# Kernel tuning notes

Hardware: AMD Instinct MI355X
Metric: run time of the kernel (lower is better)

Reference implementation:

```python
import jax, jax.numpy as jnp
import numpy as np

DIM = 256
NUM_HEADS = 4
HEAD_DIM = DIM // NUM_HEADS


def setup_inputs() -> dict:
    key = jax.random.key(0)
    ks = jax.random.split(key, 8)
    B, N, C = 4, 2048, DIM
    x = jax.random.normal(ks[0], (B, N, C), dtype=jnp.float32)
    R = jax.random.normal(ks[1], (B, 3, 3), dtype=jnp.float32)
    P = jax.random.normal(ks[2], (N, 3), dtype=jnp.float32)
    s = 1.0 / np.sqrt(C)
    qkv_w = jax.random.normal(ks[3], (3 * C, C), dtype=jnp.float32) * s
    qkv_b = jax.random.normal(ks[4], (3 * C,), dtype=jnp.float32) * 0.02
    proj_w = jax.random.normal(ks[5], (C, C), dtype=jnp.float32) * s
    proj_b = jax.random.normal(ks[6], (C,), dtype=jnp.float32) * 0.02
    pos_scale = jnp.asarray(1.0, dtype=jnp.float32)
    return {"x": x, "R": R, "P": P, "qkv_w": qkv_w, "qkv_b": qkv_b,
            "proj_w": proj_w, "proj_b": proj_b, "pos_scale": pos_scale}


def reference(x, R, P, qkv_w, qkv_b, proj_w, proj_b, pos_scale):
    B, N, C = x.shape
    H, D = NUM_HEADS, HEAD_DIM
    scale = D ** -0.5
    # qkv: (B,N,3C) -> (3,B,H,N,D)
    qkv = (x @ qkv_w.T + qkv_b).reshape(B, N, 3, H, D).transpose(2, 0, 3, 1, 4)
    q, k, v = qkv[0], qkv[1], qkv[2]
    # attention logits (B,H,N,N)
    attn = jnp.einsum('bhid,bhjd->bhij', q, k) * scale
    # positional bias: RP = (R @ P^T)^T -> (B,N,3); bias_ij = dot(RP_i, P_j)
    RP = jnp.einsum('bab,jb->bja', R, P) if False else jnp.einsum('bca,ja->bjc', jnp.swapaxes(R, 1, 2), P)
    RP = jnp.einsum('bcd,jd->bjc', R, P)  # (B,N,3): (R @ P.T).T
    bias = jnp.einsum('bik,jk->bij', RP, P)[:, None, :, :] * pos_scale  # (B,1,N,N) broadcast over heads
    attn = jax.nn.softmax(attn + bias, axis=-1)
    out = jnp.einsum('bhij,bhjd->bhid', attn, v)  # (B,H,N,D)
    out = out.transpose(0, 2, 1, 3).reshape(B, N, C)
    out = out @ proj_w.T + proj_b
    return out
```

## Files before the change

kernel.cpp:

```cpp
#include <hip/hip_runtime.h>
#include <hip/hip_bf16.h>

#define B_ 4
#define N_ 2048
#define C_ 256
#define H_ 4
#define D_ 64

typedef __attribute__((ext_vector_type(8))) short bf16x8;
typedef __attribute__((ext_vector_type(4))) float f32x4;

#define LOG2E 1.4426950408889634f

static __device__ inline unsigned short f2bf(float f) {
    unsigned u = __builtin_bit_cast(unsigned, f);
    unsigned r = (u + 0x7fffu + ((u >> 16) & 1u)) >> 16;
    return (unsigned short)r;
}
static __device__ inline float bf2f(unsigned short h) {
    unsigned u = ((unsigned)h) << 16;
    return __builtin_bit_cast(float, u);
}
static __device__ inline unsigned pack2(float a, float b) {
    __hip_bfloat162 h = __float22bfloat162_rn(make_float2(a, b));
    unsigned u;
    __builtin_memcpy(&u, &h, 4);
    return u;
}
static __device__ inline bf16x8 ld_frag(const unsigned short* p) {
    return __builtin_bit_cast(bf16x8, *(const uint4*)p);
}
static __device__ inline void gload_lds16(const unsigned short* g, unsigned short* l) {
    __builtin_amdgcn_global_load_lds(
        (const __attribute__((address_space(1))) unsigned int*)(g),
        (__attribute__((address_space(3))) unsigned int*)(l),
        16, 0, 0);
}
template<int CTRL>
static __device__ inline float fmax_dpp(float x) {
    int yi = __builtin_amdgcn_update_dpp(0, __builtin_bit_cast(int, x),
                                         CTRL, 0xf, 0xf, true);
    return fmaxf(x, __builtin_bit_cast(float, yi));
}

__global__ __launch_bounds__(256) void cvt_kernel(
    const float* __restrict__ x, const float* __restrict__ qkv_w,
    const float* __restrict__ proj_w, const float* __restrict__ Pm,
    unsigned short* __restrict__ xb, unsigned short* __restrict__ wqb,
    unsigned short* __restrict__ wpb, unsigned short* __restrict__ eb)
{
    const int bid = blockIdx.x, tid = threadIdx.x;
    if (bid >= 1152) {
        const int n = (bid - 1152) * 256 + tid;
        const float* pp = Pm + n * 3;
        float p0 = pp[0], p1 = pp[1], p2 = pp[2];
        unsigned u0 = f2bf(p0), u1 = f2bf(p1), u2 = f2bf(p2);
        unsigned v0 = f2bf(p0 - bf2f((unsigned short)u0));
        unsigned v1 = f2bf(p1 - bf2f((unsigned short)u1));
        unsigned v2 = f2bf(p2 - bf2f((unsigned short)u2));
        uint4 lo, hi;
        lo.x = u0 | (u1 << 16); lo.y = u2 | (v0 << 16);
        lo.z = v1 | (v2 << 16); lo.w = u0 | (u1 << 16);
        hi.x = u2; hi.y = 0u; hi.z = 0u; hi.w = 0u;
        *(uint4*)&eb[n * 16 + 0] = lo;
        *(uint4*)&eb[n * 16 + 8] = hi;
        return;
    }
    const float* s; unsigned short* d; int i;
    if (bid < 1024)      { s = x;      d = xb;  i = (bid * 256 + tid) * 8; }
    else if (bid < 1120) { s = qkv_w;  d = wqb; i = ((bid - 1024) * 256 + tid) * 8; }
    else                 { s = proj_w; d = wpb; i = ((bid - 1120) * 256 + tid) * 8; }
    float4 a = *(const float4*)(s + i);
    float4 b = *(const float4*)(s + i + 4);
    uint4 u;
    u.x = pack2(a.x, a.y); u.y = pack2(a.z, a.w);
    u.z = pack2(b.x, b.y); u.w = pack2(b.z, b.w);
    *(uint4*)(d + i) = u;
}

__global__ __launch_bounds__(256) void qkv_gemm(
    const unsigned short* __restrict__ xb, const unsigned short* __restrict__ wb,
    const float* __restrict__ bias, unsigned short* __restrict__ qb,
    unsigned short* __restrict__ kb, unsigned short* __restrict__ vt)
{
    __shared__ __align__(16) unsigned short As[2][128 * 64];
    __shared__ __align__(16) unsigned short Bs[2][128 * 64];
    const int m0 = blockIdx.x * 128, o0 = blockIdx.y * 128;
    const int tid = threadIdx.x;
    const int wave = tid >> 6, lane = tid & 63, quad = lane >> 4, l16 = lane & 15;
    const int wy = wave >> 1, wx = wave & 1;
    const int x7 = l16 & 7;
    const int rl = lane >> 3, sl = lane & 7;
    const int swz = (sl ^ rl) * 8;

    const unsigned short* aq0 = &xb[(size_t)(m0 + 32 * wave + rl) * 256 + swz];
    const unsigned short* bq0 = &wb[(size_t)(o0 + 32 * wave + rl) * 256 + swz];

    auto ISSUE = [&](int buf, int k0) {
        unsigned short* ad = &As[buf][(32 * wave) * 64];
        unsigned short* bd = &Bs[buf][(32 * wave) * 64];
        #pragma unroll
        for (int i = 0; i < 4; ++i) {
            gload_lds16(aq0 + (size_t)(8 * i) * 256 + k0, ad + (8 * i) * 64);
            gload_lds16(bq0 + (size_t)(8 * i) * 256 + k0, bd + (8 * i) * 64);
        }
    };

    f32x4 acc[4][4];
    #pragma unroll
    for (int i = 0; i < 4; ++i)
        #pragma unroll
        for (int j = 0; j < 4; ++j) acc[i][j] = (f32x4){0.f, 0.f, 0.f, 0.f};

    ISSUE(0, 0);

    #pragma unroll
    for (int t = 0; t < 4; ++t) {
        const int cur = t & 1;
        asm volatile("s_waitcnt vmcnt(0)" ::: "memory");
        __builtin_amdgcn_s_barrier();
        __builtin_amdgcn_sched_barrier(0);
        if (t < 3) ISSUE(cur ^ 1, (t + 1) * 64);
        __builtin_amdgcn_s_setprio(1);
        #pragma unroll
        for (int ks = 0; ks < 2; ++ks) {
            bf16x8 a[4], b[4];
            #pragma unroll
            for (int mt = 0; mt < 4; ++mt)
                a[mt] = ld_frag(&As[cur][(wy * 64 + mt * 16 + l16) * 64
                                         + (((ks * 4 + quad) ^ x7) * 8)]);
            #pragma unroll
            for (int nt = 0; nt < 4; ++nt)
                b[nt] = ld_frag(&Bs[cur][(wx * 64 + nt * 16 + l16) * 64
                                         + (((ks * 4 + quad) ^ x7) * 8)]);
            #pragma unroll
            for (int mt = 0; mt < 4; ++mt)
                #pragma unroll
                for (int nt = 0; nt < 4; ++nt)
                    acc[mt][nt] = __builtin_amdgcn_mfma_f32_16x16x32_bf16(a[mt], b[nt], acc[mt][nt], 0, 0, 0);
        }
        __builtin_amdgcn_s_setprio(0);
    }

    const int sec = o0 + wx * 64;
    const int three = sec >> 8;
    const int h = (sec >> 6) & 3;
    const int b = m0 >> 11;
    float bv[4];
    #pragma unroll
    for (int nt = 0; nt < 4; ++nt) bv[nt] = bias[sec + nt * 16 + l16];

    if (three == 2) {
        const int n64 = (m0 + wy * 64) & 2047;
        const size_t bh64 = ((size_t)b * H_ + h) * 64;
        #pragma unroll
        for (int nt = 0; nt < 4; ++nt) {
            int d = nt * 16 + l16;
            #pragma unroll
            for (int r = 0; r < 4; ++r) {
                ushort4 v;
                v.x = f2bf(acc[0][nt][r] + bv[nt]);
                v.y = f2bf(acc[1][nt][r] + bv[nt]);
                v.z = f2bf(acc[2][nt][r] + bv[nt]);
                v.w = f2bf(acc[3][nt][r] + bv[nt]);
                *(ushort4*)&vt[(bh64 + d) * N_ + n64 + 16 * quad + 4 * r] = v;
            }
        }
    } else {
        unsigned short* dst = (three == 0) ? qb : kb;
        float sc = (three == 0) ? (0.125f * LOG2E) : 1.0f;
        #pragma unroll
        for (int mt = 0; mt < 4; ++mt)
            #pragma unroll
            for (int r = 0; r < 4; ++r) {
                int n = (m0 + wy * 64 + mt * 16 + quad * 4 + r) & 2047;
                size_t rowbase = (((size_t)b * H_ + h) * N_ + n) * D_;
                #pragma unroll
                for (int nt = 0; nt < 4; ++nt)
                    dst[rowbase + nt * 16 + l16] = f2bf((acc[mt][nt][r] + bv[nt]) * sc);
            }
    }
}

#define LDK 64

__global__ __launch_bounds__(512, 4) void attn_kernel(
    const unsigned short* __restrict__ qb, const unsigned short* __restrict__ kb,
    const unsigned short* __restrict__ vt, const unsigned short* __restrict__ eb,
    const float* __restrict__ Rm, const float* __restrict__ Pm,
    const float* __restrict__ ps_ptr,
    unsigned short* __restrict__ Opart, float* __restrict__ ml)
{
    __shared__ __align__(16) unsigned short Ks[2][64 * LDK];
    __shared__ __align__(16) unsigned short Vs[2][64 * LDK];
    __shared__ __align__(16) unsigned short Ps[128 * LDK];

    const int bh = blockIdx.y;
    const int b = bh >> 2;
    const int i0 = blockIdx.x * 128;
    const int split = blockIdx.z;
    const int tid = threadIdx.x;
    const int wave = tid >> 6, lane = tid & 63;
    const int quad = lane >> 4, l16 = lane & 15;
    const int x7 = l16 & 7;
    const float ps = ps_ptr[0];

    const size_t base = (size_t)bh * N_ * D_;
    const unsigned short* qg = qb + base;
    const unsigned short* kg = kb + base;
    const unsigned short* vg = vt + base;

    const int jbeg = split * (N_ / 2);

    const int rl = lane >> 3, sl = lane & 7;
    const int swz = (sl ^ rl) * 8;
    const unsigned short* kq = kg + (size_t)(jbeg + wave * 8 + rl) * D_ + swz;
    const unsigned short* vq = vg + (size_t)(wave * 8 + rl) * N_ + jbeg + swz;
    const unsigned short* ep = eb + (size_t)(jbeg + l16) * 16 + (quad & 1) * 8;

    auto ISSUE_K = [&](int nb) {
        gload_lds16(kq, &Ks[nb][(wave * 8) * LDK]);
        kq += 64 * D_;
    };
    auto ISSUE_V = [&](int nb) {
        gload_lds16(vq, &Vs[nb][(wave * 8) * LDK]);
        vq += 64;
    };
    auto LOAD_E = [&](bf16x8 (&e)[4]) {
        #pragma unroll
        for (int t = 0; t < 4; ++t) e[t] = ld_frag(ep + t * 256);
        ep += 64 * 16;
    };

    ISSUE_K(0);
    bf16x8 eA[4], eB[4];
    LOAD_E(eA);

    const int qrow = i0 + wave * 16 + l16;
    bf16x8 aq[3];
    #pragma unroll
    for (int ks = 0; ks < 2; ++ks)
        aq[ks] = ld_frag(&qg[(size_t)qrow * D_ + ks * 32 + quad * 8]);

    {
        float p0 = Pm[qrow * 3 + 0], p1 = Pm[qrow * 3 + 1], p2 = Pm[qrow * 3 + 2];
        float sc = ps * LOG2E;
        unsigned short ah[3], al[3];
        #pragma unroll
        for (int c = 0; c < 3; ++c) {
            float a = (Rm[b * 9 + c * 3 + 0] * p0 + Rm[b * 9 + c * 3 + 1] * p1
                     + Rm[b * 9 + c * 3 + 2] * p2) * sc;
            ah[c] = f2bf(a);
            al[c] = f2bf(a - bf2f(ah[c]));
        }
        bf16x8 e = (bf16x8){0,0,0,0,0,0,0,0};
        if (quad == 0) {
            e[0] = (short)ah[0]; e[1] = (short)ah[1]; e[2] = (short)ah[2];
            e[3] = (short)ah[0]; e[4] = (short)ah[1]; e[5] = (short)ah[2];
            e[6] = (short)al[0]; e[7] = (short)al[1];
        } else if (quad == 1) {
            e[0] = (short)al[2];
        }
        aq[2] = e;
    }

    const bf16x8 ones = (bf16x8){0x3F80,0x3F80,0x3F80,0x3F80,0x3F80,0x3F80,0x3F80,0x3F80};

    float m_run = -1e30f;
    f32x4 o_acc[4], lacc;
    #pragma unroll
    for (int t = 0; t < 4; ++t) o_acc[t] = (f32x4){0.f, 0.f, 0.f, 0.f};
    lacc = (f32x4){0.f, 0.f, 0.f, 0.f};

    f32x4 sA[4], sB[4];

    auto S_COMPUTE = [&](f32x4 (&sc)[4], int kb_, bf16x8 (&ec)[4]) {
        __builtin_amdgcn_s_setprio(1);
        #pragma unroll
        for (int t = 0; t < 4; ++t) {
            const int rb = (l16 + 16 * t) * LDK;
            f32x4 c = {0.f, 0.f, 0.f, 0.f};
            #pragma unroll
            for (int ks = 0; ks < 2; ++ks) {
                bf16x8 bk = ld_frag(&Ks[kb_][rb + (((ks * 4 + quad) ^ x7) * 8)]);
                c = __builtin_amdgcn_mfma_f32_16x16x32_bf16(aq[ks], bk, c, 0, 0, 0);
            }
            c = __builtin_amdgcn_mfma_f32_16x16x32_bf16(aq[2], ec[t], c, 0, 0, 0);
            sc[t] = c;
        }
        __builtin_amdgcn_s_setprio(0);
    };

    auto SOFTMAX = [&](f32x4 (&s)[4]) {
        float mt[4];
        #pragma unroll
        for (int t = 0; t < 4; ++t)
            mt[t] = fmaxf(fmaxf(fmaxf(s[t][0], s[t][1]), s[t][2]), s[t][3]);
        float mx = fmaxf(fmaxf(fmaxf(mt[0], mt[1]), mt[2]), mt[3]);
        mx = fmax_dpp<0xB1>(mx);
        mx = fmax_dpp<0x4E>(mx);
        mx = fmax_dpp<0x124>(mx);
        mx = fmax_dpp<0x128>(mx);
        if (__any(mx > m_run + 8.0f)) {
            float mnew = fmaxf(m_run, mx);
            float alpha = exp2f(m_run - mnew);
            #pragma unroll
            for (int t = 0; t < 4; ++t)
                #pragma unroll
                for (int r = 0; r < 4; ++r)
                    o_acc[t][r] *= alpha;
            #pragma unroll
            for (int r = 0; r < 4; ++r) lacc[r] *= alpha;
            m_run = mnew;
        }
        #pragma unroll
        for (int r = 0; r < 4; ++r) {
            float p0 = exp2f(s[0][r] - m_run), p1 = exp2f(s[1][r] - m_run);
            float p2 = exp2f(s[2][r] - m_run), p3 = exp2f(s[3][r] - m_run);
            uint2 w;
            w.x = pack2(p0, p1);
            w.y = pack2(p2, p3);
            const int prow = quad * 4 + r;
            *(uint2*)&Ps[(wave * 16 + prow) * LDK
                         + (((l16 >> 1) ^ (prow & 7)) * 8) + (l16 & 1) * 4] = w;
        }
    };

    auto PV = [&](int vb_) {
        __builtin_amdgcn_s_setprio(1);
        #pragma unroll
        for (int ks = 0; ks < 2; ++ks) {
            bf16x8 ap = ld_frag(&Ps[(wave * 16 + l16) * LDK
                                    + (((ks * 4 + quad) ^ x7) * 8)]);
            #pragma unroll
            for (int t = 0; t < 4; ++t) {
                bf16x8 bv = ld_frag(&Vs[vb_][(l16 + 16 * t) * LDK
                                             + (((ks * 4 + quad) ^ x7) * 8)]);
                o_acc[t] = __builtin_amdgcn_mfma_f32_16x16x32_bf16(ap, bv, o_acc[t], 0, 0, 0);
            }
            lacc = __builtin_amdgcn_mfma_f32_16x16x32_bf16(ap, ones, lacc, 0, 0, 0);
        }
        __builtin_amdgcn_s_setprio(0);
    };

    auto STEP = [&](int cur, bool more, f32x4 (&snew)[4], f32x4 (&sold)[4],
                    bf16x8 (&euse)[4], bf16x8 (&eload)[4]) {
        asm volatile("s_waitcnt vmcnt(0)" ::: "memory");
        __builtin_amdgcn_s_barrier();
        __builtin_amdgcn_sched_barrier(0);
        if (more) ISSUE_K(cur ^ 1);
        ISSUE_V(cur);
        SOFTMAX(sold);
        S_COMPUTE(snew, cur, euse);
        if (more) LOAD_E(eload);
        PV(cur ^ 1);
    };

    asm volatile("s_waitcnt vmcnt(0)" ::: "memory");
    __builtin_amdgcn_s_barrier();
    __builtin_amdgcn_sched_barrier(0);
    ISSUE_K(1);
    ISSUE_V(0);
    S_COMPUTE(sA, 0, eA);
    LOAD_E(eB);

    #pragma unroll 1
    for (int it = 0; it < 7; ++it) {
        STEP(1, true, sB, sA, eB, eA);
        STEP(0, true, sA, sB, eA, eB);
    }
    STEP(1, false, sB, sA, eB, eA);

    asm volatile("s_waitcnt vmcnt(0)" ::: "memory");
    __builtin_amdgcn_s_barrier();
    __builtin_amdgcn_sched_barrier(0);
    SOFTMAX(sB);
    PV(1);

    const size_t pbase = (size_t)(split * 16 + bh) * N_;
    #pragma unroll
    for (int r = 0; r < 4; ++r) {
        int row = i0 + wave * 16 + quad * 4 + r;
        #pragma unroll
        for (int t = 0; t < 4; ++t)
            Opart[(pbase + row) * D_ + l16 + 16 * t] = f2bf(o_acc[t][r]);
        if (l16 == 0) {
            float2* mlp = (float2*)ml;
            mlp[pbase + row] = make_float2(m_run, lacc[r]);
        }
    }
}

__global__ __launch_bounds__(256) void proj_gemm(
    const unsigned short* __restrict__ Opart, const float* __restrict__ ml,
    const unsigned short* __restrict__ wb, const float* __restrict__ bias,
    float* __restrict__ out)
{
    __shared__ __align__(16) unsigned short As[2][64 * 64];
    __shared__ __align__(16) unsigned short Bs[2][64 * 64];
    const int m0 = blockIdx.x * 64, o0 = blockIdx.y * 64;
    const int tid = threadIdx.x;
    const int wave = tid >> 6, lane = tid & 63, quad = lane >> 4, l16 = lane & 15;
    const int x7 = l16 & 7;
    const int rl = lane >> 3, sl = lane & 7;
    const int swz = (sl ^ rl) * 8;
    const float2* mlp = (const float2*)ml;

    const int srow = tid >> 2, sc16 = (tid & 3) * 16;
    const int s0 = (tid & 3) * 2;
    const int sm = m0 + srow, sb = sm >> 11, sn = sm & 2047;

    float wgt[4][2];
    #pragma unroll
    for (int h = 0; h < 4; ++h) {
        size_t r1 = (size_t)(sb * 4 + h) * N_ + sn;
        float2 m0v = mlp[r1], m1v = mlp[r1 + 16 * N_];
        float mm = fmaxf(m0v.x, m1v.x);
        float w0 = exp2f(m0v.x - mm), w1 = exp2f(m1v.x - mm);
        float inv = 1.f / (m0v.y * w0 + m1v.y * w1);
        wgt[h][0] = w0 * inv; wgt[h][1] = w1 * inv;
    }

    const unsigned short* bq0 = &wb[(size_t)(o0 + 16 * wave + rl) * 256 + swz];
    auto ISSUE_B = [&](int buf, int k0) {
        unsigned short* bd = &Bs[buf][(16 * wave) * 64];
        gload_lds16(bq0 + k0,           bd);
        gload_lds16(bq0 + 8 * 256 + k0, bd + 8 * 64);
    };

    union U16 { uint4 u; unsigned short s[8]; };
    U16 ar[2][2];
    auto LOAD_A = [&](int h) {
        size_t r1 = (size_t)(sb * 4 + h) * N_ + sn;
        #pragma unroll
        for (int s = 0; s < 2; ++s) {
            const unsigned short* p = &Opart[(r1 + (size_t)(16 * s) * N_) * D_ + sc16];
            ar[s][0].u = *(const uint4*)(p);
            ar[s][1].u = *(const uint4*)(p + 8);
        }
    };

    ISSUE_B(0, 0);
    LOAD_A(0);

    f32x4 acc[4];
    #pragma unroll
    for (int j = 0; j < 4; ++j) acc[j] = (f32x4){0.f, 0.f, 0.f, 0.f};

    #pragma unroll
    for (int t = 0; t < 4; ++t) {
        const int cur = t & 1;
        {
            float w0 = wgt[t][0], w1 = wgt[t][1];
            #pragma unroll
            for (int j = 0; j < 2; ++j) {
                uint4 mv;
                unsigned* mp = (unsigned*)&mv;
                #pragma unroll
                for (int q = 0; q < 4; ++q) {
                    float lo = bf2f(ar[0][j].s[2*q])   * w0 + bf2f(ar[1][j].s[2*q])   * w1;
                    float hi = bf2f(ar[0][j].s[2*q+1]) * w0 + bf2f(ar[1][j].s[2*q+1]) * w1;
                    mp[q] = pack2(lo, hi);
                }
                *(uint4*)&As[cur][srow * 64 + (((s0 + j) ^ (srow & 7)) * 8)] = mv;
            }
        }
        __syncthreads();
        if (t < 3) {
            ISSUE_B(cur ^ 1, (t + 1) * 64);
            LOAD_A(t + 1);
        }
        __builtin_amdgcn_s_setprio(1);
        #pragma unroll
        for (int ks = 0; ks < 2; ++ks) {
            bf16x8 a = ld_frag(&As[cur][(wave * 16 + l16) * 64
                                        + (((ks * 4 + quad) ^ x7) * 8)]);
            #pragma unroll
            for (int nt = 0; nt < 4; ++nt) {
                bf16x8 b = ld_frag(&Bs[cur][(nt * 16 + l16) * 64
                                            + (((ks * 4 + quad) ^ x7) * 8)]);
                acc[nt] = __builtin_amdgcn_mfma_f32_16x16x32_bf16(a, b, acc[nt], 0, 0, 0);
            }
        }
        __builtin_amdgcn_s_setprio(0);
    }

    float bv[4];
    #pragma unroll
    for (int nt = 0; nt < 4; ++nt) bv[nt] = bias[o0 + nt * 16 + l16];
    #pragma unroll
    for (int r = 0; r < 4; ++r) {
        int m = m0 + wave * 16 + quad * 4 + r;
        #pragma unroll
        for (int nt = 0; nt < 4; ++nt)
            out[(size_t)m * 256 + o0 + nt * 16 + l16] = acc[nt][r] + bv[nt];
    }
}

extern "C" void kernel_launch(void* const* d_in, const int* in_sizes, int n_in,
                              void* d_out, int out_size, void* d_ws, size_t ws_size,
                              hipStream_t stream) {
    const float* x       = (const float*)d_in[0];
    const float* Rm      = (const float*)d_in[1];
    const float* Pm      = (const float*)d_in[2];
    const float* qkv_w   = (const float*)d_in[3];
    const float* qkv_b   = (const float*)d_in[4];
    const float* proj_w  = (const float*)d_in[5];
    const float* proj_b  = (const float*)d_in[6];
    const float* pos_scl = (const float*)d_in[7];
    float* out = (float*)d_out;

    const size_t NE = (size_t)B_ * H_ * N_ * D_;
    unsigned short* opart = (unsigned short*)d_ws;
    unsigned short* qb    = opart + 2 * NE;
    unsigned short* kb    = qb   + NE;
    unsigned short* vtb   = kb   + NE;
    float*          mlb   = (float*)(vtb + NE);
    unsigned short* eb    = (unsigned short*)(mlb + (size_t)2 * 16 * N_ * 2);
    unsigned short* wqb   = eb  + 2048 * 16;
    unsigned short* wpb   = wqb + 768 * 256;
    unsigned short* xb    = opart;

    cvt_kernel<<<1160, 256, 0, stream>>>(x, qkv_w, proj_w, Pm, xb, wqb, wpb, eb);
    qkv_gemm<<<dim3(64, 6), 256, 0, stream>>>(xb, wqb, qkv_b, qb, kb, vtb);
    attn_kernel<<<dim3(16, 16, 2), 512, 0, stream>>>(qb, kb, vtb, eb, Rm, Pm, pos_scl, opart, mlb);
    proj_gemm<<<dim3(128, 4), 256, 0, stream>>>(opart, mlb, wpb, proj_b, out);
}
```

Before: 127.0 us.

## Keep softmax probabilities in registers via transposed S MFMA and lane shuffles

Swaps the MFMA operand order for the QK^T scores so each lane holds a transposed score fragment. The P fragments for the PV MFMA are then built with cross-lane shuffles instead of going through the shared-memory Ps buffer. This drops the LDS write and read per step and frees 16KB of shared memory. In exchange it adds shuffle and select instructions. The max reduction now spans the whole wave and no longer takes a per-row max, which gives up precision headroom only within the existing threshold of 8.

```diff
diff --git a/kernel.cpp b/kernel.cpp
--- a/kernel.cpp
+++ b/kernel.cpp
@@ -193,7 +193,6 @@
 {
     __shared__ __align__(16) unsigned short Ks[2][64 * LDK];
     __shared__ __align__(16) unsigned short Vs[2][64 * LDK];
-    __shared__ __align__(16) unsigned short Ps[128 * LDK];
 
     const int bh = blockIdx.y;
     const int b = bh >> 2;
@@ -283,27 +282,28 @@
             #pragma unroll
             for (int ks = 0; ks < 2; ++ks) {
                 bf16x8 bk = ld_frag(&Ks[kb_][rb + (((ks * 4 + quad) ^ x7) * 8)]);
-                c = __builtin_amdgcn_mfma_f32_16x16x32_bf16(aq[ks], bk, c, 0, 0, 0);
-            }
-            c = __builtin_amdgcn_mfma_f32_16x16x32_bf16(aq[2], ec[t], c, 0, 0, 0);
+                c = __builtin_amdgcn_mfma_f32_16x16x32_bf16(bk, aq[ks], c, 0, 0, 0);
+            }
+            c = __builtin_amdgcn_mfma_f32_16x16x32_bf16(ec[t], aq[2], c, 0, 0, 0);
             sc[t] = c;
         }
         __builtin_amdgcn_s_setprio(0);
     };
 
-    auto SOFTMAX = [&](f32x4 (&s)[4]) {
-        float mt[4];
+    auto SOFTMAX_X = [&](f32x4 (&s)[4], bf16x8 &ap0, bf16x8 &ap1) {
+        float mt4[4];
         #pragma unroll
         for (int t = 0; t < 4; ++t)
-            mt[t] = fmaxf(fmaxf(fmaxf(s[t][0], s[t][1]), s[t][2]), s[t][3]);
-        float mx = fmaxf(fmaxf(fmaxf(mt[0], mt[1]), mt[2]), mt[3]);
+            mt4[t] = fmaxf(fmaxf(fmaxf(s[t][0], s[t][1]), s[t][2]), s[t][3]);
+        float mx = fmaxf(fmaxf(fmaxf(mt4[0], mt4[1]), mt4[2]), mt4[3]);
         mx = fmax_dpp<0xB1>(mx);
         mx = fmax_dpp<0x4E>(mx);
         mx = fmax_dpp<0x124>(mx);
         mx = fmax_dpp<0x128>(mx);
-        if (__any(mx > m_run + 8.0f)) {
-            float mnew = fmaxf(m_run, mx);
-            float alpha = exp2f(m_run - mnew);
+        mx = fmaxf(mx, __shfl_xor(mx, 16));
+        mx = fmaxf(mx, __shfl_xor(mx, 32));
+        if (mx > m_run + 8.0f) {
+            float alpha = exp2f(m_run - mx);
             #pragma unroll
             for (int t = 0; t < 4; ++t)
                 #pragma unroll
@@ -311,27 +311,45 @@
                     o_acc[t][r] *= alpha;
             #pragma unroll
             for (int r = 0; r < 4; ++r) lacc[r] *= alpha;
-            m_run = mnew;
-        }
+            m_run = mx;
+        }
+        unsigned W[4][2];
         #pragma unroll
         for (int r = 0; r < 4; ++r) {
             float p0 = exp2f(s[0][r] - m_run), p1 = exp2f(s[1][r] - m_run);
             float p2 = exp2f(s[2][r] - m_run), p3 = exp2f(s[3][r] - m_run);
-            uint2 w;
-            w.x = pack2(p0, p1);
-            w.y = pack2(p2, p3);
-            const int prow = quad * 4 + r;
-            *(uint2*)&Ps[(wave * 16 + prow) * LDK
-                         + (((l16 >> 1) ^ (prow & 7)) * 8) + (l16 & 1) * 4] = w;
-        }
-    };
-
-    auto PV = [&](int vb_) {
+            W[r][0] = pack2(p0, p1);
+            W[r][1] = pack2(p2, p3);
+        }
+        const bool q01 = (quad < 2);
+        const bool q1s = (quad == 1);
+        unsigned a16[4], a32[4], a48[4];
+        #pragma unroll
+        for (int a = 0; a < 2; ++a)
+            #pragma unroll
+            for (int h = 0; h < 2; ++h) {
+                const int i = a * 2 + h;
+                a16[i] = (unsigned)__shfl_xor((int)(q01 ? W[2 + a][h] : W[a][h]), 16);
+                a32[i] = (unsigned)__shfl_xor((int)(q1s ? W[2 + a][h] : W[a][h]), 32);
+                a48[i] = (unsigned)__shfl_xor((int)(q1s ? W[a][h] : W[2 + a][h]), 48);
+            }
+        uint4 slo, shi, v16, v32, v48;
+        slo.x = W[0][0]; slo.y = W[0][1]; slo.z = W[1][0]; slo.w = W[1][1];
+        shi.x = W[2][0]; shi.y = W[2][1]; shi.z = W[3][0]; shi.w = W[3][1];
+        v16.x = a16[0]; v16.y = a16[1]; v16.z = a16[2]; v16.w = a16[3];
+        v32.x = a32[0]; v32.y = a32[1]; v32.z = a32[2]; v32.w = a32[3];
+        v48.x = a48[0]; v48.y = a48[1]; v48.z = a48[2]; v48.w = a48[3];
+        uint4 w0 = (quad == 0) ? slo : (quad == 1) ? v16 : (quad == 2) ? v48 : v32;
+        uint4 w1 = (quad == 0) ? v32 : (quad == 1) ? v48 : (quad == 2) ? v16 : shi;
+        ap0 = __builtin_bit_cast(bf16x8, w0);
+        ap1 = __builtin_bit_cast(bf16x8, w1);
+    };
+
+    auto PV = [&](int vb_, bf16x8 ap0, bf16x8 ap1) {
         __builtin_amdgcn_s_setprio(1);
         #pragma unroll
         for (int ks = 0; ks < 2; ++ks) {
-            bf16x8 ap = ld_frag(&Ps[(wave * 16 + l16) * LDK
-                                    + (((ks * 4 + quad) ^ x7) * 8)]);
+            bf16x8 ap = ks ? ap1 : ap0;
             #pragma unroll
             for (int t = 0; t < 4; ++t) {
                 bf16x8 bv = ld_frag(&Vs[vb_][(l16 + 16 * t) * LDK
@@ -350,10 +368,11 @@
         __builtin_amdgcn_sched_barrier(0);
         if (more) ISSUE_K(cur ^ 1);
         ISSUE_V(cur);
-        SOFTMAX(sold);
+        bf16x8 ap0, ap1;
+        SOFTMAX_X(sold, ap0, ap1);
         S_COMPUTE(snew, cur, euse);
         if (more) LOAD_E(eload);
-        PV(cur ^ 1);
+        PV(cur ^ 1, ap0, ap1);
     };
 
     asm volatile("s_waitcnt vmcnt(0)" ::: "memory");
@@ -374,8 +393,11 @@
     asm volatile("s_waitcnt vmcnt(0)" ::: "memory");
     __builtin_amdgcn_s_barrier();
     __builtin_amdgcn_sched_barrier(0);
-    SOFTMAX(sB);
-    PV(1);
+    {
+        bf16x8 ap0, ap1;
+        SOFTMAX_X(sB, ap0, ap1);
+        PV(1, ap0, ap1);
+    }
 
     const size_t pbase = (size_t)(split * 16 + bh) * N_;
     #pragma unroll
```

Result: slower. 171.8 us (+35.3%).
